# Performance work log

Measured on AMD Instinct MI355X. Metric: run time of the kernel, lower is better.

The kernel has to match this reference:

```python
import jax, jax.numpy as jnp
import numpy as np

EULER = 0.5772156649015329  # Euler-Mascheroni constant


def _expi_neg(t):
    """Ei(t) for t < 0, via Ei(t) = -E1(-t).

    E1 uses the power series for x < 8 and the asymptotic expansion for x >= 8.
    This replaces the scipy.special.expi CPU round-trip of the original module.
    """
    x = -t  # x > 0
    # --- series branch (x < 8): E1(x) = -gamma - ln(x) + sum_{k>=1} (-1)^{k+1} x^k/(k*k!)
    xs = jnp.minimum(x, 8.0)
    s = jnp.zeros_like(xs)
    term = xs  # (-1)^{k+1} xs^k / k!  starting at k=1
    for k in range(1, 31):
        s = s + term / k
        term = term * (-xs) / (k + 1)
    e1_small = -EULER - jnp.log(xs) + s
    # --- asymptotic branch (x >= 8): E1(x) ~ e^{-x}/x * sum_n (-1)^n n! / x^n
    xl = jnp.maximum(x, 8.0)
    a = jnp.ones_like(xl)
    acc = jnp.ones_like(xl)
    for n in range(1, 9):
        a = a * (-n) / xl
        acc = acc + a
    e1_large = jnp.exp(-xl) / xl * acc
    e1 = jnp.where(x < 8.0, e1_small, e1_large)
    return -e1


def _li(v):
    # logarithmic integral li(v) = Ei(ln v); constant w.r.t. params (scipy detaches in torch)
    return jax.lax.stop_gradient(_expi_neg(jnp.log(v)))


def _phi(u, var2, var3, var4, var5):
    log_term = jnp.log(1.0 - u)
    li_term = _li(1.0 - u)
    return (var2 / log_term
            + var3 * li_term
            + var4 * ((1.0 - u) / log_term - li_term)
            + var5 * ((1.0 - u) * (log_term + 1.0) / (2.0 * log_term ** 2) - li_term / 2.0))


def setup_inputs() -> dict:
    key = jax.random.key(0)
    B, L, D = 262144, 64, 32
    hidden = [128, 128, 64]
    ks = jax.random.split(key, 16)
    u = jax.random.uniform(ks[0], (B, L), dtype=jnp.float32, minval=1e-4, maxval=1.0 - 1e-4)
    dims = [L] + hidden + [D]
    inp = {"u": u}
    for i in range(4):
        inp[f"W{i}"] = jax.random.normal(ks[1 + 2 * i], (dims[i], dims[i + 1]), dtype=jnp.float32) / np.sqrt(dims[i]).astype(np.float32)
        inp[f"b{i}"] = jnp.zeros((dims[i + 1],), dtype=jnp.float32)
    for j in range(1, 7):
        inp[f"var{j}"] = jax.random.normal(ks[8 + j], (1, D), dtype=jnp.float32) * 0.1
    return inp


def reference(u, W0, b0, W1, b1, W2, b2, W3, b3, var1, var2, var3, var4, var5, var6):
    # MLP: three Linear+ReLU blocks then final Linear to dim_data
    h = u
    for W, b in ((W0, b0), (W1, b1), (W2, b2)):
        h = jax.nn.relu(h @ W + b)
    net = h @ W3 + b3  # (B, dim_data)
    D = net.shape[1]
    ud = u[:, :D]
    # spline corrections
    p01 = -4.0 * ud ** 5 + 5.0 * ud ** 4
    corr1 = jnp.nan_to_num(p01 * (var1 + _phi(ud, var2, var3, var4, var5)), nan=0.0)
    corr2 = var6 * (ud ** 3 - 2.0 * ud ** 2 + ud)
    net_tif = jax.nn.relu(net + corr1 + corr2)
    # inverse TIF activation: ((1 - u^2)/2)^{-x}
    return jnp.power((1.0 - ud ** 2) / 2.0, -net_tif)
```

## Files before the change

### kernel.cpp

```cpp
#include <hip/hip_runtime.h>
#include <hip/hip_bf16.h>
#include <math.h>

#define LN2_F 0.69314718055994531f
#define INV_LN2_F 1.44269504088896341f
#define REGION_HALFS 2048

typedef _Float16 half8 __attribute__((ext_vector_type(8)));
typedef _Float16 h4_t __attribute__((ext_vector_type(4)));
typedef __fp16 pk2_t __attribute__((ext_vector_type(2)));
typedef __attribute__((ext_vector_type(4))) float f32x4;
typedef __attribute__((ext_vector_type(8))) short short8;

#define MFMA16(a, b, c) __builtin_amdgcn_mfma_f32_16x16x32_f16((a), (b), (c), 0, 0, 0)

__global__ void prep_weights(const float* __restrict__ W0, const float* __restrict__ W1,
                             const float* __restrict__ W2, const float* __restrict__ W3,
                             short* __restrict__ ws) {
    int e = blockIdx.x * 256 + threadIdx.x;
    const float* W; int N, NT, base, ul;
    if (e < 1024)      { W = W0; N = 128; NT = 8; base = 0;     ul = e; }
    else if (e < 3072) { W = W1; N = 128; NT = 8; base = 8192;  ul = e - 1024; }
    else if (e < 4096) { W = W2; N = 64;  NT = 4; base = 24576; ul = e - 3072; }
    else if (e < 4352) { W = W3; N = 32;  NT = 2; base = 32768; ul = e - 4096; }
    else return;
    const int cp = ul >> 6, lane = ul & 63;
    const int s = cp / NT, ct = cp % NT;
    const int k0 = s * 32 + (lane >> 4) * 8;
    const int n = ct * 16 + (lane & 15);
    union { half8 h; short8 s; } v;
#pragma unroll
    for (int j = 0; j < 8; ++j) v.h[j] = (_Float16)W[(size_t)(k0 + j) * N + n];
    *(short8*)(ws + base + cp * 512 + lane * 8) = v.s;
}


__device__ __forceinline__ void lds_fence() {
    asm volatile("s_waitcnt lgkmcnt(0)" ::: "memory");
}

__device__ __forceinline__ half8 tr_read_ks(const _Float16* region, unsigned lane_off, int s) {
    h4_t lo, hi;
    asm volatile("ds_read_b64_tr_b16 %0, %2\n\t"
                 "ds_read_b64_tr_b16 %1, %2 offset:128"
                 : "=&v"(lo), "=&v"(hi)
                 : "v"((unsigned)(uintptr_t)region + lane_off + (unsigned)(s * 1024))
                 : "memory");
    return __builtin_shufflevector(lo, hi, 0, 1, 2, 3, 4, 5, 6, 7);
}

__device__ __forceinline__ void store_tile(_Float16* __restrict__ region, int ct_global,
                                           int m, int q, f32x4 v) {
    const int base = ct_global * 256 + (m >> 2) * 64 + (m & 3) * 16 + q * 4;
    pk2_t p0 = __builtin_amdgcn_cvt_pkrtz(v[0], v[1]);
    pk2_t p1 = __builtin_amdgcn_cvt_pkrtz(v[2], v[3]);
    h4_t h = {(_Float16)p0[0], (_Float16)p0[1], (_Float16)p1[0], (_Float16)p1[1]};
    h = __builtin_elementwise_max(h, (h4_t)(_Float16)0.0f);
    *(h4_t*)(region + base) = h;
}

template <int NK, int NT, int NC>
__device__ __forceinline__ void layer_half(const half8* __restrict__ wf,
                                           const float* __restrict__ bias, int ct0,
                                           const half8 (&af)[2][4], int lane, int m,
                                           f32x4 (&acc)[2][4]) {
#pragma unroll
    for (int c = 0; c < NC; ++c) {
        const float b = bias[(ct0 + c) * 16 + m];
        acc[0][c] = f32x4{b, b, b, b};
        acc[1][c] = f32x4{b, b, b, b};
    }
#pragma unroll
    for (int s = 0; s < NK; ++s) {
        half8 bf[4];
#pragma unroll
        for (int c = 0; c < NC; ++c) bf[c] = wf[(s * NT + ct0 + c) * 64 + lane];
#pragma unroll
        for (int c = 0; c < NC; ++c) {
            acc[0][c] = MFMA16(af[0][s], bf[c], acc[0][c]);
            acc[1][c] = MFMA16(af[1][s], bf[c], acc[1][c]);
        }
    }
}

__global__ __launch_bounds__(256, 4) void mlp_phi_mfma(
    const float* __restrict__ u,
    const float* __restrict__ b0, const float* __restrict__ b1,
    const float* __restrict__ b2, const float* __restrict__ b3,
    const short* __restrict__ ws,
    const float* __restrict__ var1, const float* __restrict__ var2,
    const float* __restrict__ var3, const float* __restrict__ var4,
    const float* __restrict__ var5, const float* __restrict__ var6,
    float* __restrict__ out) {
    __shared__ __align__(16) _Float16 lds[4 * 2 * REGION_HALFS];
    const int t = threadIdx.x, lane = t & 63, wave = t >> 6;
    const int m = lane & 15, q = lane >> 4;
    _Float16* lw = lds + wave * 2 * REGION_HALFS;
    const unsigned lane_rd = (unsigned)(q * 256 + m * 8);
    const size_t row0 = (size_t)blockIdx.x * 128 + wave * 32;

    const half8* wf0 = (const half8*)(ws);
    const half8* wf1 = (const half8*)(ws + 8192);
    const half8* wf2 = (const half8*)(ws + 24576);
    const half8* wf3 = (const half8*)(ws + 32768);

    half8 af[2][4];
    f32x4 acc[2][4];

#pragma unroll
    for (int mt = 0; mt < 2; ++mt) {
        const float* up = u + (row0 + mt * 16 + m) * 64;
#pragma unroll
        for (int s = 0; s < 2; ++s) {
            float4 v0a = *(const float4*)(up + s * 32 + q * 8);
            float4 v1a = *(const float4*)(up + s * 32 + q * 8 + 4);
            pk2_t p0 = __builtin_amdgcn_cvt_pkrtz(v0a.x, v0a.y);
            pk2_t p1 = __builtin_amdgcn_cvt_pkrtz(v0a.z, v0a.w);
            pk2_t p2 = __builtin_amdgcn_cvt_pkrtz(v1a.x, v1a.y);
            pk2_t p3 = __builtin_amdgcn_cvt_pkrtz(v1a.z, v1a.w);
            af[mt][s] = half8{(_Float16)p0[0], (_Float16)p0[1], (_Float16)p1[0], (_Float16)p1[1],
                              (_Float16)p2[0], (_Float16)p2[1], (_Float16)p3[0], (_Float16)p3[1]};
        }
    }

#pragma unroll
    for (int h = 0; h < 2; ++h) {
        layer_half<2, 8, 4>(wf0, b0, h * 4, af, lane, m, acc);
#pragma unroll
        for (int mt = 0; mt < 2; ++mt)
#pragma unroll
            for (int cc = 0; cc < 4; ++cc)
                store_tile(lw + mt * REGION_HALFS, h * 4 + cc, m, q, acc[mt][cc]);
    }
    lds_fence();
#pragma unroll
    for (int mt = 0; mt < 2; ++mt)
#pragma unroll
        for (int s = 0; s < 4; ++s) af[mt][s] = tr_read_ks(lw + mt * REGION_HALFS, lane_rd, s);
    lds_fence();
    __builtin_amdgcn_sched_barrier(0);

#pragma unroll
    for (int h = 0; h < 2; ++h) {
        layer_half<4, 8, 4>(wf1, b1, h * 4, af, lane, m, acc);
#pragma unroll
        for (int mt = 0; mt < 2; ++mt)
#pragma unroll
            for (int cc = 0; cc < 4; ++cc)
                store_tile(lw + mt * REGION_HALFS, h * 4 + cc, m, q, acc[mt][cc]);
    }
    lds_fence();
#pragma unroll
    for (int mt = 0; mt < 2; ++mt)
#pragma unroll
        for (int s = 0; s < 4; ++s) af[mt][s] = tr_read_ks(lw + mt * REGION_HALFS, lane_rd, s);
    lds_fence();
    __builtin_amdgcn_sched_barrier(0);

    layer_half<4, 4, 4>(wf2, b2, 0, af, lane, m, acc);
#pragma unroll
    for (int mt = 0; mt < 2; ++mt)
#pragma unroll
        for (int cc = 0; cc < 4; ++cc)
            store_tile(lw + mt * REGION_HALFS, cc, m, q, acc[mt][cc]);
    lds_fence();
#pragma unroll
    for (int mt = 0; mt < 2; ++mt)
#pragma unroll
        for (int s = 0; s < 2; ++s) af[mt][s] = tr_read_ks(lw + mt * REGION_HALFS, lane_rd, s);

    float ue[2][8];
#pragma unroll
    for (int mt = 0; mt < 2; ++mt)
#pragma unroll
        for (int ot = 0; ot < 2; ++ot)
#pragma unroll
            for (int r = 0; r < 4; ++r)
                ue[mt][ot * 4 + r] = u[(row0 + mt * 16 + q * 4 + r) * 64 + ot * 16 + m];

    lds_fence();
    __builtin_amdgcn_sched_barrier(0);

    layer_half<2, 2, 2>(wf3, b3, 0, af, lane, m, acc);

#pragma unroll
    for (int ot = 0; ot < 2; ++ot) {
        const int d = ot * 16 + m;
        const float v1 = var1[d], v6 = var6[d];
        const float v2p = var2[d] * INV_LN2_F;
        const float v4 = var4[d];
        const float v4p = v4 * INV_LN2_F;
        const float v5h = 0.5f * var5[d];
        const float v5hp = v5h * INV_LN2_F;
        const float c3 = var3[d] - v4 - v5h;
#pragma unroll
        for (int mt = 0; mt < 2; ++mt) {
#pragma unroll
            for (int r = 0; r < 4; ++r) {
                const size_t row = row0 + mt * 16 + q * 4 + r;
                const float net = acc[mt][ot][r];
                const float ud = ue[mt][ot * 4 + r];

                const float omu = 1.0f - ud;
                const float L = __log2f(omu);
                const float x = -L * LN2_F;
                const float RL = __builtin_amdgcn_rcpf(L);

                const float e1s = -__log2f(x) * LN2_F
                    + (-0.57721566f + x * (0.99999193f + x * (-0.24991055f
                    + x * (0.05519968f + x * (-0.00976004f + x * 0.00107857f)))));
                const float num = 0.2677737343f + x * (8.6347608925f + x * (18.0590169730f
                    + x * (8.5733287401f + x)));
                const float den = 3.9584969228f + x * (21.0996530827f + x * (25.6329561486f
                    + x * (9.5733223454f + x)));
                const float e1l = omu * num * __builtin_amdgcn_rcpf(x * den);
                const float li = -((x < 1.0f) ? e1s : e1l);

                const float phi = fmaf(v4p, omu, v2p) * RL
                                + (v5hp * omu * (L + INV_LN2_F)) * RL * RL
                                + c3 * li;

                const float ud2 = ud * ud;
                const float ud4 = ud2 * ud2;
                const float p01 = ud4 * fmaf(-4.0f, ud, 5.0f);
                const float corr1 = p01 * (v1 + phi);
                const float d1 = ud - 1.0f;
                const float corr2 = v6 * ud * d1 * d1;

                const float nt = fmaxf(net + corr1 + corr2, 0.0f);
                const float base = fmaf(-0.5f, ud2, 0.5f);
                out[row * 32 + d] = __builtin_amdgcn_exp2f(-nt * __log2f(base));
            }
        }
    }
}

extern "C" void kernel_launch(void* const* d_in, const int* in_sizes, int n_in,
                              void* d_out, int out_size, void* d_ws, size_t ws_size,
                              hipStream_t stream) {
    const float* u    = (const float*)d_in[0];
    const float* W0   = (const float*)d_in[1];
    const float* b0   = (const float*)d_in[2];
    const float* W1   = (const float*)d_in[3];
    const float* b1   = (const float*)d_in[4];
    const float* W2   = (const float*)d_in[5];
    const float* b2   = (const float*)d_in[6];
    const float* W3   = (const float*)d_in[7];
    const float* b3   = (const float*)d_in[8];
    const float* var1 = (const float*)d_in[9];
    const float* var2 = (const float*)d_in[10];
    const float* var3 = (const float*)d_in[11];
    const float* var4 = (const float*)d_in[12];
    const float* var5 = (const float*)d_in[13];
    const float* var6 = (const float*)d_in[14];
    float* out = (float*)d_out;
    short* ws = (short*)d_ws;

    prep_weights<<<dim3(17), dim3(256), 0, stream>>>(W0, W1, W2, W3, ws);

    const int B = in_sizes[0] / 64;
    const int blocks = B / 128;
    mlp_phi_mfma<<<dim3(blocks), dim3(256), 0, stream>>>(
        u, b0, b1, b2, b3, ws,
        var1, var2, var3, var4, var5, var6, out);
}
```

Measured before the change: 150.9 us.

## Stream MLP weight fragments into LDS ring via async global_load_lds pipeline

Replaces per-wave direct global loads of weight fragments with a three-slot LDS ring that wave 0 fills using asynchronous global_load_lds two stages ahead. All four waves then read the shared fragments from LDS, with block barriers at each stage. Bias values are also preloaded into registers up front. The aim is to cut redundant global/L2 weight traffic and hide its latency, at the cost of 17 block-wide barriers and extra LDS use that may lower occupancy.

```diff
diff --git a/kernel.cpp b/kernel.cpp
--- a/kernel.cpp
+++ b/kernel.cpp
@@ -5,6 +5,7 @@
 #define LN2_F 0.69314718055994531f
 #define INV_LN2_F 1.44269504088896341f
 #define REGION_HALFS 2048
+#define SLOT_SH 2048
 
 typedef _Float16 half8 __attribute__((ext_vector_type(8)));
 typedef _Float16 h4_t __attribute__((ext_vector_type(4)));
@@ -34,7 +35,6 @@
     *(short8*)(ws + base + cp * 512 + lane * 8) = v.s;
 }
 
-
 __device__ __forceinline__ void lds_fence() {
     asm volatile("s_waitcnt lgkmcnt(0)" ::: "memory");
 }
@@ -59,29 +59,68 @@
     *(h4_t*)(region + base) = h;
 }
 
-template <int NK, int NT, int NC>
-__device__ __forceinline__ void layer_half(const half8* __restrict__ wf,
-                                           const float* __restrict__ bias, int ct0,
-                                           const half8 (&af)[2][4], int lane, int m,
-                                           f32x4 (&acc)[2][4]) {
-#pragma unroll
-    for (int c = 0; c < NC; ++c) {
-        const float b = bias[(ct0 + c) * 16 + m];
-        acc[0][c] = f32x4{b, b, b, b};
-        acc[1][c] = f32x4{b, b, b, b};
-    }
-#pragma unroll
-    for (int s = 0; s < NK; ++s) {
-        half8 bf[4];
-#pragma unroll
-        for (int c = 0; c < NC; ++c) bf[c] = wf[(s * NT + ct0 + c) * 64 + lane];
-#pragma unroll
-        for (int c = 0; c < NC; ++c) {
-            acc[0][c] = MFMA16(af[0][s], bf[c], acc[0][c]);
-            acc[1][c] = MFMA16(af[1][s], bf[c], acc[1][c]);
-        }
-    }
-}
+__device__ __forceinline__ void gll_frag(const short* g, short* l) {
+    __builtin_amdgcn_global_load_lds(
+        (const __attribute__((address_space(1))) void*)g,
+        (__attribute__((address_space(3))) void*)l, 16, 0, 0);
+}
+
+template <int N>
+__device__ __forceinline__ void wait_vmcnt() {
+    asm volatile("s_waitcnt vmcnt(%0)" :: "n"(N) : "memory");
+}
+
+__device__ __forceinline__ void stage4(const short* wl, int fb, short* slot, int lane8) {
+#pragma unroll
+    for (int c = 0; c < 4; ++c)
+        gll_frag(wl + (size_t)(fb + c) * 512 + lane8, slot + c * 512);
+}
+
+#define PIPE_STAGE(k)                                                              \
+    do { if (wave == 0 && (k) + 2 <= 16)                                           \
+        stage4(sp[(k) + 2], sfb[(k) + 2], ring + (((k) + 2) % 3) * SLOT_SH, lane8);\
+    } while (0)
+
+#define PIPE_END(k)                                                                \
+    do {                                                                           \
+        if (wave == 0) {                                                           \
+            if ((k) + 2 <= 16) wait_vmcnt<4>();              \
+            else wait_vmcnt<0>();                          \
+        }                                                                          \
+        __builtin_amdgcn_sched_barrier(0);                                         \
+        __builtin_amdgcn_s_barrier();                                              \
+        __builtin_amdgcn_sched_barrier(0);                                         \
+    } while (0)
+
+#define ACC_INIT(bb, o)                                                            \
+    do { _Pragma("unroll") for (int c = 0; c < 4; ++c) {                           \
+        const float b_ = (bb)[(o) + c];                                            \
+        acc[0][c] = f32x4{b_, b_, b_, b_};                                         \
+        acc[1][c] = f32x4{b_, b_, b_, b_};                                         \
+    } } while (0)
+
+#define CONSUME(k, sidx)                                                           \
+    do { const short* slot_ = ring + ((k) % 3) * SLOT_SH;                          \
+        _Pragma("unroll") for (int c = 0; c < 4; ++c) {                            \
+            half8 b_ = *(const half8*)(slot_ + c * 512 + lane8);                   \
+            acc[0][c] = MFMA16(af[0][sidx], b_, acc[0][c]);                        \
+            acc[1][c] = MFMA16(af[1][sidx], b_, acc[1][c]);                        \
+        } } while (0)
+
+#define STORE_HALF(ct0)                                                            \
+    do { _Pragma("unroll") for (int mt = 0; mt < 2; ++mt)                          \
+        _Pragma("unroll") for (int cc = 0; cc < 4; ++cc)                           \
+            store_tile(lw + mt * REGION_HALFS, (ct0) + cc, m, q, acc[mt][cc]);     \
+    } while (0)
+
+#define TRANS(KS)                                                                  \
+    do { lds_fence();                                                              \
+        _Pragma("unroll") for (int mt = 0; mt < 2; ++mt)                           \
+            _Pragma("unroll") for (int s_ = 0; s_ < (KS); ++s_)                    \
+                af[mt][s_] = tr_read_ks(lw + mt * REGION_HALFS, lane_rd, s_);      \
+        lds_fence();                                                               \
+        __builtin_amdgcn_sched_barrier(0);                                         \
+    } while (0)
 
 __global__ __launch_bounds__(256, 4) void mlp_phi_mfma(
     const float* __restrict__ u,
@@ -92,17 +131,34 @@
     const float* __restrict__ var3, const float* __restrict__ var4,
     const float* __restrict__ var5, const float* __restrict__ var6,
     float* __restrict__ out) {
-    __shared__ __align__(16) _Float16 lds[4 * 2 * REGION_HALFS];
+    __shared__ __align__(16) _Float16 act[4 * 2 * REGION_HALFS];
+    __shared__ __align__(16) short ring[3 * SLOT_SH];
+
     const int t = threadIdx.x, lane = t & 63, wave = t >> 6;
     const int m = lane & 15, q = lane >> 4;
-    _Float16* lw = lds + wave * 2 * REGION_HALFS;
+    const int lane8 = lane * 8;
+    _Float16* lw = act + wave * 2 * REGION_HALFS;
     const unsigned lane_rd = (unsigned)(q * 256 + m * 8);
     const size_t row0 = (size_t)blockIdx.x * 128 + wave * 32;
 
-    const half8* wf0 = (const half8*)(ws);
-    const half8* wf1 = (const half8*)(ws + 8192);
-    const half8* wf2 = (const half8*)(ws + 24576);
-    const half8* wf3 = (const half8*)(ws + 32768);
+    const short* wl0 = ws;
+    const short* wl1 = ws + 8192;
+    const short* wl2 = ws + 24576;
+    const short* wl3 = ws + 32768;
+
+    const short* const sp[17] = {wl0, wl0, wl0, wl0,  wl1, wl1, wl1, wl1,
+                                 wl1, wl1, wl1, wl1,  wl2, wl2, wl2, wl2,  wl3};
+    const int sfb[17] = {0, 8, 4, 12,  0, 8, 16, 24,  4, 12, 20, 28,  0, 4, 8, 12,  0};
+
+    float bb0v[8], bb1v[8], bb2v[4], bb3v[2];
+#pragma unroll
+    for (int ct = 0; ct < 8; ++ct) bb0v[ct] = b0[ct * 16 + m];
+#pragma unroll
+    for (int ct = 0; ct < 8; ++ct) bb1v[ct] = b1[ct * 16 + m];
+#pragma unroll
+    for (int ct = 0; ct < 4; ++ct) bb2v[ct] = b2[ct * 16 + m];
+#pragma unroll
+    for (int ct = 0; ct < 2; ++ct) bb3v[ct] = b3[ct * 16 + m];
 
     half8 af[2][4];
     f32x4 acc[2][4];
@@ -122,52 +178,33 @@
                               (_Float16)p2[0], (_Float16)p2[1], (_Float16)p3[0], (_Float16)p3[1]};
         }
     }
-
-#pragma unroll
-    for (int h = 0; h < 2; ++h) {
-        layer_half<2, 8, 4>(wf0, b0, h * 4, af, lane, m, acc);
-#pragma unroll
-        for (int mt = 0; mt < 2; ++mt)
-#pragma unroll
-            for (int cc = 0; cc < 4; ++cc)
-                store_tile(lw + mt * REGION_HALFS, h * 4 + cc, m, q, acc[mt][cc]);
+    if (wave == 0) {
+        stage4(sp[0], sfb[0], ring, lane8);
+        stage4(sp[1], sfb[1], ring + SLOT_SH, lane8);
+        wait_vmcnt<4>();
     }
-    lds_fence();
-#pragma unroll
-    for (int mt = 0; mt < 2; ++mt)
-#pragma unroll
-        for (int s = 0; s < 4; ++s) af[mt][s] = tr_read_ks(lw + mt * REGION_HALFS, lane_rd, s);
-    lds_fence();
     __builtin_amdgcn_sched_barrier(0);
-
-#pragma unroll
-    for (int h = 0; h < 2; ++h) {
-        layer_half<4, 8, 4>(wf1, b1, h * 4, af, lane, m, acc);
-#pragma unroll
-        for (int mt = 0; mt < 2; ++mt)
-#pragma unroll
-            for (int cc = 0; cc < 4; ++cc)
-                store_tile(lw + mt * REGION_HALFS, h * 4 + cc, m, q, acc[mt][cc]);
-    }
-    lds_fence();
-#pragma unroll
-    for (int mt = 0; mt < 2; ++mt)
-#pragma unroll
-        for (int s = 0; s < 4; ++s) af[mt][s] = tr_read_ks(lw + mt * REGION_HALFS, lane_rd, s);
-    lds_fence();
+    __builtin_amdgcn_s_barrier();
     __builtin_amdgcn_sched_barrier(0);
 
-    layer_half<4, 4, 4>(wf2, b2, 0, af, lane, m, acc);
-#pragma unroll
-    for (int mt = 0; mt < 2; ++mt)
-#pragma unroll
-        for (int cc = 0; cc < 4; ++cc)
-            store_tile(lw + mt * REGION_HALFS, cc, m, q, acc[mt][cc]);
-    lds_fence();
-#pragma unroll
-    for (int mt = 0; mt < 2; ++mt)
-#pragma unroll
-        for (int s = 0; s < 2; ++s) af[mt][s] = tr_read_ks(lw + mt * REGION_HALFS, lane_rd, s);
+    PIPE_STAGE(0); ACC_INIT(bb0v, 0); CONSUME(0, 0); PIPE_END(0);
+    PIPE_STAGE(1); CONSUME(1, 1); STORE_HALF(0); PIPE_END(1);
+    PIPE_STAGE(2); ACC_INIT(bb0v, 4); CONSUME(2, 0); PIPE_END(2);
+    PIPE_STAGE(3); CONSUME(3, 1); STORE_HALF(4); TRANS(4); PIPE_END(3);
+
+    PIPE_STAGE(4); ACC_INIT(bb1v, 0); CONSUME(4, 0); PIPE_END(4);
+    PIPE_STAGE(5); CONSUME(5, 1); PIPE_END(5);
+    PIPE_STAGE(6); CONSUME(6, 2); PIPE_END(6);
+    PIPE_STAGE(7); CONSUME(7, 3); STORE_HALF(0); PIPE_END(7);
+    PIPE_STAGE(8); ACC_INIT(bb1v, 4); CONSUME(8, 0); PIPE_END(8);
+    PIPE_STAGE(9); CONSUME(9, 1); PIPE_END(9);
+    PIPE_STAGE(10); CONSUME(10, 2); PIPE_END(10);
+    PIPE_STAGE(11); CONSUME(11, 3); STORE_HALF(4); TRANS(4); PIPE_END(11);
+
+    PIPE_STAGE(12); ACC_INIT(bb2v, 0); CONSUME(12, 0); PIPE_END(12);
+    PIPE_STAGE(13); CONSUME(13, 1); PIPE_END(13);
+    PIPE_STAGE(14); CONSUME(14, 2); PIPE_END(14);
+    PIPE_STAGE(15); CONSUME(15, 3); STORE_HALF(0); TRANS(2); PIPE_END(15);
 
     float ue[2][8];
 #pragma unroll
@@ -177,11 +214,23 @@
 #pragma unroll
             for (int r = 0; r < 4; ++r)
                 ue[mt][ot * 4 + r] = u[(row0 + mt * 16 + q * 4 + r) * 64 + ot * 16 + m];
-
-    lds_fence();
-    __builtin_amdgcn_sched_barrier(0);
-
-    layer_half<2, 2, 2>(wf3, b3, 0, af, lane, m, acc);
+    {
+        const short* slot_ = ring + (16 % 3) * SLOT_SH;
+#pragma unroll
+        for (int c = 0; c < 2; ++c) {
+            const float b_ = bb3v[c];
+            acc[0][c] = f32x4{b_, b_, b_, b_};
+            acc[1][c] = f32x4{b_, b_, b_, b_};
+        }
+#pragma unroll
+        for (int s = 0; s < 2; ++s)
+#pragma unroll
+            for (int c = 0; c < 2; ++c) {
+                half8 b_ = *(const half8*)(slot_ + (s * 2 + c) * 512 + lane8);
+                acc[0][c] = MFMA16(af[0][s], b_, acc[0][c]);
+                acc[1][c] = MFMA16(af[1][s], b_, acc[1][c]);
+            }
+    }
 
 #pragma unroll
     for (int ot = 0; ot < 2; ++ot) {
```

Result: no change. 153.6 us (+1.8%).
